# Performance work log

Measured on AMD Instinct MI355X. Metric: run time of the kernel, lower is better.

Reference implementation:

```python
import jax, jax.numpy as jnp
import numpy as np


def c2p_gather(feat, ind):
    # feat: [B, C, M] cell features; ind: [B, N, 2] (slot 0 = cell index)
    B, C, _ = feat.shape
    idx = ind[:, :, 0]                                   # [B, N]
    idx3 = jnp.broadcast_to(idx[:, None, :], (B, C, idx.shape[1]))
    return jnp.take_along_axis(feat, idx3, axis=2)       # [B, C, N]


def p2c_scatter(x, ind, num_cells):
    # x: [B, C, Nn] point features; ind: [B, Nn, 2]; scatter-add into [B, C, M]
    idx = ind[:, :, 0]                                   # [B, Nn]

    def per_batch(xb, ib):
        # xb: [C, Nn] -> segment_sum over points -> [M, C]
        return jax.ops.segment_sum(xb.T, ib, num_segments=num_cells).T

    return jax.vmap(per_batch)(x, idx)                   # [B, C, M]


def setup_inputs() -> dict:
    key = jax.random.key(0)
    ks = jax.random.split(key, 8)
    B, Cv, Cr, E, Co = 2, 64, 20, 64, 64
    Mv, Mr = 100000, 50000
    N = 262144            # gathered points; os=8 -> bundle=4 -> Nn=65536 nodes
    Nn = N // 4
    return {
        "v_feat": jax.random.normal(ks[0], (B, Cv, Mv), jnp.float32),
        "r_feat": jax.random.normal(ks[1], (B, Cr, Mr), jnp.float32),
        "Wq": jax.random.normal(ks[2], (E, Cr), jnp.float32) * 0.1,
        "Wk": jax.random.normal(ks[3], (E, Cv), jnp.float32) * 0.1,
        "Wv": jax.random.normal(ks[4], (E, Cv), jnp.float32) * 0.1,
        "Wo": jax.random.normal(ks[5], (Co, E), jnp.float32) * 0.1,
        "v2p_ind": jax.random.randint(ks[6], (B, N, 2), 0, Mv).astype(jnp.int64),
        "r2p_ind": jax.random.randint(ks[7], (B, Nn, 2), 0, Mr).astype(jnp.int64),
        "os": 8,
    }


def reference(v_feat, r_feat, Wq, Wk, Wv, Wo, v2p_ind, r2p_ind, os):
    bundle = max(1, int(os) // 2)
    B, Cv, _ = v_feat.shape
    Mr = r_feat.shape[2]

    # c2p gather of detached features (module calls .detach())
    v_pp = c2p_gather(jax.lax.stop_gradient(v_feat), v2p_ind)       # [B, Cv, N]
    N = v_pp.shape[2]
    Nn = N // bundle
    v_nodes = v_pp.reshape(B, Cv, Nn, bundle)                        # bundle splits
    r_pp = c2p_gather(jax.lax.stop_gradient(r_feat), r2p_ind)        # [B, Cr, Nn]

    # attent1d: query from r feature, keys/values from the neighbor bundle
    E = Wq.shape[0]
    q = jnp.einsum("ec,bcn->ben", Wq, r_pp)                          # [B, E, Nn]
    k = jnp.einsum("ec,bcnm->benm", Wk, v_nodes)                     # [B, E, Nn, bundle]
    v = jnp.einsum("ec,bcnm->benm", Wv, v_nodes)
    scores = jnp.einsum("ben,benm->bnm", q, k) / jnp.sqrt(jnp.float32(E))
    attn = jax.nn.softmax(scores, axis=-1)                           # over bundle
    agg = jnp.einsum("bnm,benm->ben", attn, v)                       # [B, E, Nn]
    xr = jnp.einsum("oe,ben->bon", Wo, agg)                          # [B, Co, Nn]

    # p2c scatter back to r-cell layout (size taken from r_feat)
    xr_mapped = p2c_scatter(xr, r2p_ind, Mr)                         # [B, Co, Mr]
    return xr_mapped
```

## Files before the change

kernel.cpp:

```cpp
#include <hip/hip_runtime.h>
#include <cstdint>

#define BB 2
#define CV 64
#define CR 20
#define EE 64
#define CO 64
#define NZ 256

__global__ __launch_bounds__(256) void k_tr(
    const float* __restrict__ vf, float* __restrict__ vt, int Mv, int ntm) {
  __shared__ float tile[64 * 64];
  int b = blockIdx.x / ntm, tm = blockIdx.x % ntm;
  int m0 = tm * 64;
  int t = threadIdx.x;
  const float* src = vf + (size_t)b * CV * Mv;
  float* dst = vt + (size_t)b * Mv * 64;
  if (((Mv & 3) == 0) && (m0 + 64 <= Mv)) {
    #pragma unroll
    for (int p = 0; p < 4; ++p) {
      int c = p * 16 + (t >> 4), mq = t & 15;
      float4 v = *(const float4*)&src[(size_t)c * Mv + m0 + 4 * mq];
      *(float4*)&tile[c * 64 + ((mq ^ ((c >> 2) & 15)) << 2)] = v;
    }
    __syncthreads();
    #pragma unroll
    for (int p = 0; p < 4; ++p) {
      int ml = p * 16 + (t >> 4), cq = t & 15;
      int mc = ml >> 2, mr = ml & 3;
      int ch = (mc ^ cq) << 2;
      float4 w;
      w.x = tile[(4 * cq + 0) * 64 + ch + mr];
      w.y = tile[(4 * cq + 1) * 64 + ch + mr];
      w.z = tile[(4 * cq + 2) * 64 + ch + mr];
      w.w = tile[(4 * cq + 3) * 64 + ch + mr];
      *(float4*)&dst[(size_t)(m0 + ml) * 64 + 4 * cq] = w;
    }
  } else {
    for (int p = 0; p < 16; ++p) {
      int idx = p * 256 + t;
      int c = idx >> 6, ml = idx & 63;
      int m = m0 + ml;
      float v = (m < Mv) ? src[(size_t)c * Mv + m] : 0.f;
      tile[c * 64 + (((ml >> 2) ^ ((c >> 2) & 15)) << 2) + (ml & 3)] = v;
    }
    __syncthreads();
    for (int p = 0; p < 16; ++p) {
      int idx = p * 256 + t;
      int ml = idx >> 6, c = idx & 63;
      int m = m0 + ml;
      if (m < Mv)
        dst[(size_t)m * 64 + c] =
            tile[c * 64 + (((ml >> 2) ^ ((c >> 2) & 15)) << 2) + (ml & 3)];
    }
  }
}

__global__ __launch_bounds__(256) void k_pre(
    const float* __restrict__ rf,
    const float* __restrict__ Wq, const float* __restrict__ Wk,
    const float* __restrict__ Wv, const float* __restrict__ Wo,
    const int* __restrict__ r2p,
    float* __restrict__ gq, float* __restrict__ H,
    int* __restrict__ flag, float4* __restrict__ xs4,
    int Mr, int ntj, int NGQ, int xsE4) {
  __shared__ float smem[CR * 64 + CR * 68];
  int bid = blockIdx.x, t = threadIdx.x;
  if (bid < NGQ) {
    float* Gl = smem;
    float* rt = smem + CR * 64;
    for (int idx = t; idx < CR * CV; idx += 256) {
      int cr = idx / CV, cv = idx - cr * CV;
      float s = 0.f;
      #pragma unroll
      for (int e = 0; e < EE; ++e) s += Wq[e * CR + cr] * Wk[e * CV + cv];
      Gl[idx] = s;
    }
    int b = bid / ntj, tj = bid - b * ntj;
    int j0 = tj * 64;
    const float* src = rf + (size_t)b * CR * Mr;
    for (int idx = t; idx < CR * 64; idx += 256) {
      int c = idx >> 6, jl = idx & 63;
      int j = j0 + jl;
      rt[c * 68 + jl] = (j < Mr) ? src[(size_t)c * Mr + j] : 0.f;
    }
    __syncthreads();
    int ti = t & 15, tjq = t >> 4;
    float acc[4][4];
    #pragma unroll
    for (int a = 0; a < 4; ++a)
      #pragma unroll
      for (int q = 0; q < 4; ++q) acc[a][q] = 0.f;
    for (int c = 0; c < CR; ++c) {
      float4 gx = *(const float4*)&Gl[c * 64 + 4 * ti];
      float4 xj = *(const float4*)&rt[c * 68 + 4 * tjq];
      #pragma unroll
      for (int a = 0; a < 4; ++a) {
        float xv = (a == 0) ? xj.x : (a == 1) ? xj.y : (a == 2) ? xj.z : xj.w;
        acc[a][0] += xv * gx.x;
        acc[a][1] += xv * gx.y;
        acc[a][2] += xv * gx.z;
        acc[a][3] += xv * gx.w;
      }
    }
    #pragma unroll
    for (int a = 0; a < 4; ++a) {
      int j = j0 + 4 * tjq + a;
      if (j < Mr) {
        float4 w = make_float4(acc[a][0], acc[a][1], acc[a][2], acc[a][3]);
        *(float4*)&gq[((size_t)b * Mr + j) * 64 + 4 * ti] = w;
      }
    }
    return;
  }
  int r = bid - NGQ;
  if (r < 16) {
    int idx = r * 256 + t;
    int o = idx >> 6, c = idx & 63;
    float s = 0.f;
    #pragma unroll
    for (int e = 0; e < EE; ++e) s += Wo[o * EE + e] * Wv[e * CV + c];
    H[idx] = s;
  } else if (r == 16) {
    __shared__ int any;
    if (t == 0) any = 0;
    __syncthreads();
    int nz = 0;
    for (int i = t; i < 4096; i += 256) nz |= r2p[2 * i + 1];
    if (nz) atomicOr(&any, 1);
    __syncthreads();
    if (t == 0) *flag = (any == 0) ? 4 : 2;
  } else {
    int z = r - 17;
    float4 zz = make_float4(0.f, 0.f, 0.f, 0.f);
    for (int i = z * 256 + t; i < xsE4; i += NZ * 256) xs4[i] = zz;
  }
}

template <int WS>
__device__ __forceinline__ void load_idx(
    const int* __restrict__ r2p, const int* __restrict__ v2p,
    int p, int Nn, int N, int P,
    int& b, int& j, int& i0, int& i1, int& i2, int& i3) {
  if (p >= P) { b = 0; j = 0; i0 = i1 = i2 = i3 = 0; return; }
  b = (p >= Nn) ? 1 : 0;
  int n = p - b * Nn;
  j = r2p[((size_t)b * Nn + n) * WS];
  const int* vi = v2p + ((size_t)b * N + (size_t)n * 4) * WS;
  if (WS == 2) {
    int4 w0 = *(const int4*)vi;
    int4 w1 = *(const int4*)(vi + 4);
    i0 = w0.x; i1 = w0.z; i2 = w1.x; i3 = w1.z;
  } else {
    i0 = vi[0]; i1 = vi[1 * WS]; i2 = vi[2 * WS]; i3 = vi[3 * WS];
  }
}

__device__ __forceinline__ float gred16(float h) {
  h += __shfl_xor(h, 1);
  h += __shfl_xor(h, 2);
  h += __shfl_xor(h, 4);
  h += __shfl_xor(h, 8);
  return h;
}

__device__ __forceinline__ float4 att4(float4 q4, float4 c0, float4 c1,
                                       float4 c2, float4 c3) {
  float s0 = gred16(q4.x * c0.x + q4.y * c0.y + q4.z * c0.z + q4.w * c0.w);
  float s1 = gred16(q4.x * c1.x + q4.y * c1.y + q4.z * c1.z + q4.w * c1.w);
  float s2 = gred16(q4.x * c2.x + q4.y * c2.y + q4.z * c2.z + q4.w * c2.w);
  float s3 = gred16(q4.x * c3.x + q4.y * c3.y + q4.z * c3.z + q4.w * c3.w);
  s0 *= 0.125f; s1 *= 0.125f; s2 *= 0.125f; s3 *= 0.125f;
  float mx = fmaxf(fmaxf(s0, s1), fmaxf(s2, s3));
  float e0 = __expf(s0 - mx), e1 = __expf(s1 - mx);
  float e2 = __expf(s2 - mx), e3 = __expf(s3 - mx);
  float inv = 1.f / (e0 + e1 + e2 + e3);
  e0 *= inv; e1 *= inv; e2 *= inv; e3 *= inv;
  float4 ag;
  ag.x = e0 * c0.x + e1 * c1.x + e2 * c2.x + e3 * c3.x;
  ag.y = e0 * c0.y + e1 * c1.y + e2 * c2.y + e3 * c3.y;
  ag.z = e0 * c0.z + e1 * c1.z + e2 * c2.z + e3 * c3.z;
  ag.w = e0 * c0.w + e1 * c1.w + e2 * c2.w + e3 * c3.w;
  return ag;
}

template <int WS>
__device__ __forceinline__ void main_body(
    const float* __restrict__ vt, const float* __restrict__ gq,
    const int* __restrict__ v2p, const int* __restrict__ r2p,
    float* __restrict__ xs, float* __restrict__ my,
    int Mv, int Mr, int N, int Nn, int P) {
  int t = threadIdx.x;
  int lane = t & 63, sl = t & 15, grp = (t >> 4) & 3;
  int base = (blockIdx.x * 4 + (t >> 6)) * 8;
  if (base >= P) return;
  int pA = base + grp, pB = base + grp + 4;
  int bA, jA, a0, a1, a2, a3, bB, jB, b0, b1, b2, b3;
  load_idx<WS>(r2p, v2p, pA, Nn, N, P, bA, jA, a0, a1, a2, a3);
  load_idx<WS>(r2p, v2p, pB, Nn, N, P, bB, jB, b0, b1, b2, b3);
  const float* gqA = gq + (size_t)bA * Mr * 64;
  const float* vbA = vt + (size_t)bA * Mv * 64;
  const float* gqB = gq + (size_t)bB * Mr * 64;
  const float* vbB = vt + (size_t)bB * Mv * 64;
  float4 qA  = *(const float4*)&gqA[(size_t)jA * 64 + 4 * sl];
  float4 cA0 = *(const float4*)&vbA[(size_t)a0 * 64 + 4 * sl];
  float4 cA1 = *(const float4*)&vbA[(size_t)a1 * 64 + 4 * sl];
  float4 cA2 = *(const float4*)&vbA[(size_t)a2 * 64 + 4 * sl];
  float4 cA3 = *(const float4*)&vbA[(size_t)a3 * 64 + 4 * sl];
  float4 qB  = *(const float4*)&gqB[(size_t)jB * 64 + 4 * sl];
  float4 cB0 = *(const float4*)&vbB[(size_t)b0 * 64 + 4 * sl];
  float4 cB1 = *(const float4*)&vbB[(size_t)b1 * 64 + 4 * sl];
  float4 cB2 = *(const float4*)&vbB[(size_t)b2 * 64 + 4 * sl];
  float4 cB3 = *(const float4*)&vbB[(size_t)b3 * 64 + 4 * sl];
  float4 agA = att4(qA, cA0, cA1, cA2, cA3);
  *(float4*)&my[grp * 68 + 4 * sl] = agA;
  float4 agB = att4(qB, cB0, cB1, cB2, cB3);
  *(float4*)&my[(grp + 4) * 68 + 4 * sl] = agB;
  #pragma unroll
  for (int g = 0; g < 8; ++g) {
    if (base + g < P) {
      int jg = __shfl((g < 4) ? jA : jB, (g & 3) * 16);
      int bg = ((base + g) >= Nn) ? 1 : 0;
      float v = my[g * 68 + lane];
      atomicAdd(&xs[((size_t)bg * Mr + jg) * 64 + lane], v);
    }
  }
}

__global__ __launch_bounds__(256, 8) void k_main(
    const float* __restrict__ vt, const float* __restrict__ gq,
    const int* __restrict__ v2p, const int* __restrict__ r2p,
    float* __restrict__ xs, const int* __restrict__ flag,
    int Mv, int Mr, int N, int Nn, int P) {
  __shared__ float sc[4 * 8 * 68];
  float* my = sc + (threadIdx.x >> 6) * (8 * 68);
  if (*flag == 2)
    main_body<2>(vt, gq, v2p, r2p, xs, my, Mv, Mr, N, Nn, P);
  else
    main_body<4>(vt, gq, v2p, r2p, xs, my, Mv, Mr, N, Nn, P);
}

__device__ __forceinline__ int hsw(int fidx) {
  return fidx ^ (((fidx >> 8) & 7) << 2);
}

__global__ __launch_bounds__(256) void k_out_t(
    const float* __restrict__ xs, const float* __restrict__ H,
    float* __restrict__ out, int Mr, int ntj) {
  __shared__ float Hl[CO * CV];
  __shared__ float xt[64][68];
  int b = blockIdx.x / ntj, tj = blockIdx.x % ntj;
  int j0 = tj * 64;
  int t = threadIdx.x;
  for (int idx = t; idx < CO * CV; idx += 256) Hl[hsw(idx)] = H[idx];
  const float* src = xs + (size_t)b * Mr * 64;
  #pragma unroll
  for (int k = 0; k < 4; ++k) {
    int jl = k * 16 + (t >> 4), c4 = t & 15;
    int j = j0 + jl;
    float4 v = (j < Mr) ? *(const float4*)&src[(size_t)j * 64 + 4 * c4]
                        : make_float4(0.f, 0.f, 0.f, 0.f);
    *(float4*)&xt[jl][4 * c4] = v;
  }
  __syncthreads();
  int ti = t & 15;
  int tjq4 = t >> 4;
  float acc[4][4];
  #pragma unroll
  for (int a = 0; a < 4; ++a)
    #pragma unroll
    for (int q = 0; q < 4; ++q) acc[a][q] = 0.f;
  #pragma unroll 4
  for (int cq = 0; cq < 16; ++cq) {
    float4 xv[4], hb[4];
    #pragma unroll
    for (int a = 0; a < 4; ++a)
      xv[a] = *(const float4*)&xt[4 * tjq4 + a][4 * cq];
    #pragma unroll
    for (int q = 0; q < 4; ++q) {
      int row = 4 * ti + q;
      hb[q] = *(const float4*)&Hl[hsw(row * 64 + 4 * cq)];
    }
    #pragma unroll
    for (int a = 0; a < 4; ++a)
      #pragma unroll
      for (int q = 0; q < 4; ++q)
        acc[a][q] += xv[a].x * hb[q].x + xv[a].y * hb[q].y +
                     xv[a].z * hb[q].z + xv[a].w * hb[q].w;
  }
  __syncthreads();
  #pragma unroll
  for (int a = 0; a < 4; ++a)
    #pragma unroll
    for (int q = 0; q < 4; ++q)
      xt[4 * ti + q][4 * tjq4 + a] = acc[a][q];
  __syncthreads();
  float* dst = out + (size_t)b * CO * Mr;
  #pragma unroll
  for (int k = 0; k < 4; ++k) {
    int o = k * 16 + (t >> 4), j4 = t & 15;
    int j = j0 + 4 * j4;
    if (j + 3 < Mr) {
      *(float4*)&dst[(size_t)o * Mr + j] = *(const float4*)&xt[o][4 * j4];
    } else {
      #pragma unroll
      for (int i = 0; i < 4; ++i)
        if (j + i < Mr) dst[(size_t)o * Mr + j + i] = xt[o][4 * j4 + i];
    }
  }
}

extern "C" void kernel_launch(void* const* d_in, const int* in_sizes, int n_in,
                              void* d_out, int out_size, void* d_ws, size_t ws_size,
                              hipStream_t stream) {
  const float* v_feat = (const float*)d_in[0];
  const float* r_feat = (const float*)d_in[1];
  const float* Wq = (const float*)d_in[2];
  const float* Wk = (const float*)d_in[3];
  const float* Wv = (const float*)d_in[4];
  const float* Wo = (const float*)d_in[5];
  const int* v2p = (const int*)d_in[6];
  const int* r2p = (const int*)d_in[7];

  int Mv = in_sizes[0] / (BB * CV);
  int Mr = in_sizes[1] / (BB * CR);
  int N  = in_sizes[6] / (BB * 2);
  int Nn = in_sizes[7] / (BB * 2);

  float* ws = (float*)d_ws;
  float* vt = ws;
  float* gq = vt + (size_t)BB * Mv * 64;
  float* xs = gq + (size_t)BB * Mr * 64;
  float* H  = xs + (size_t)BB * Mr * 64;
  int* flag = (int*)(H + CO * CV);
  float* out = (float*)d_out;

  int ntm = (Mv + 63) / 64;
  int ntj = (Mr + 63) / 64;
  int NGQ = BB * ntj;
  int xsE4 = (BB * Mr * 64) / 4;

  k_tr<<<BB * ntm, 256, 0, stream>>>(v_feat, vt, Mv, ntm);

  k_pre<<<NGQ + 17 + NZ, 256, 0, stream>>>(r_feat, Wq, Wk, Wv, Wo, r2p,
                                           gq, H, flag, (float4*)xs,
                                           Mr, ntj, NGQ, xsE4);

  int P = BB * Nn;
  int blocks = (P + 31) / 32;
  k_main<<<blocks, 256, 0, stream>>>(vt, gq, v2p, r2p, xs, flag,
                                     Mv, Mr, N, Nn, P);

  k_out_t<<<BB * ntj, 256, 0, stream>>>(xs, H, out, Mr, ntj);
}
```

Before: 220.8 us.

## Compute Wq·Wk product once and merge weight prep into transpose kernel

The Wq^T·Wk product G was previously recomputed inside every gq block (each block did 1280 dot products of length 64). It is now computed once by a few extra blocks of the transpose kernel, along with H, the flag and the zeroing of xs. The gq projection moves to a separate lightweight kernel that only loads the precomputed G. This removes redundant per-block weight math but adds one kernel launch and one more global round trip for G.

```diff
diff --git a/kernel.cpp b/kernel.cpp
--- a/kernel.cpp
+++ b/kernel.cpp
@@ -9,119 +9,77 @@
 #define NZ 256
 
 __global__ __launch_bounds__(256) void k_tr(
-    const float* __restrict__ vf, float* __restrict__ vt, int Mv, int ntm) {
+    const float* __restrict__ vf, const float* __restrict__ Wq,
+    const float* __restrict__ Wk, const float* __restrict__ Wv,
+    const float* __restrict__ Wo, const int* __restrict__ r2p,
+    float* __restrict__ vt, float* __restrict__ G, float* __restrict__ H,
+    int* __restrict__ flag, float4* __restrict__ xs4,
+    int Mv, int ntm, int NT, int xsE4) {
   __shared__ float tile[64 * 64];
-  int b = blockIdx.x / ntm, tm = blockIdx.x % ntm;
-  int m0 = tm * 64;
-  int t = threadIdx.x;
-  const float* src = vf + (size_t)b * CV * Mv;
-  float* dst = vt + (size_t)b * Mv * 64;
-  if (((Mv & 3) == 0) && (m0 + 64 <= Mv)) {
-    #pragma unroll
-    for (int p = 0; p < 4; ++p) {
-      int c = p * 16 + (t >> 4), mq = t & 15;
-      float4 v = *(const float4*)&src[(size_t)c * Mv + m0 + 4 * mq];
-      *(float4*)&tile[c * 64 + ((mq ^ ((c >> 2) & 15)) << 2)] = v;
-    }
-    __syncthreads();
-    #pragma unroll
-    for (int p = 0; p < 4; ++p) {
-      int ml = p * 16 + (t >> 4), cq = t & 15;
-      int mc = ml >> 2, mr = ml & 3;
-      int ch = (mc ^ cq) << 2;
-      float4 w;
-      w.x = tile[(4 * cq + 0) * 64 + ch + mr];
-      w.y = tile[(4 * cq + 1) * 64 + ch + mr];
-      w.z = tile[(4 * cq + 2) * 64 + ch + mr];
-      w.w = tile[(4 * cq + 3) * 64 + ch + mr];
-      *(float4*)&dst[(size_t)(m0 + ml) * 64 + 4 * cq] = w;
-    }
-  } else {
-    for (int p = 0; p < 16; ++p) {
-      int idx = p * 256 + t;
-      int c = idx >> 6, ml = idx & 63;
-      int m = m0 + ml;
-      float v = (m < Mv) ? src[(size_t)c * Mv + m] : 0.f;
-      tile[c * 64 + (((ml >> 2) ^ ((c >> 2) & 15)) << 2) + (ml & 3)] = v;
-    }
-    __syncthreads();
-    for (int p = 0; p < 16; ++p) {
-      int idx = p * 256 + t;
-      int ml = idx >> 6, c = idx & 63;
-      int m = m0 + ml;
-      if (m < Mv)
-        dst[(size_t)m * 64 + c] =
-            tile[c * 64 + (((ml >> 2) ^ ((c >> 2) & 15)) << 2) + (ml & 3)];
-    }
-  }
-}
-
-__global__ __launch_bounds__(256) void k_pre(
-    const float* __restrict__ rf,
-    const float* __restrict__ Wq, const float* __restrict__ Wk,
-    const float* __restrict__ Wv, const float* __restrict__ Wo,
-    const int* __restrict__ r2p,
-    float* __restrict__ gq, float* __restrict__ H,
-    int* __restrict__ flag, float4* __restrict__ xs4,
-    int Mr, int ntj, int NGQ, int xsE4) {
-  __shared__ float smem[CR * 64 + CR * 68];
   int bid = blockIdx.x, t = threadIdx.x;
-  if (bid < NGQ) {
-    float* Gl = smem;
-    float* rt = smem + CR * 64;
-    for (int idx = t; idx < CR * CV; idx += 256) {
+  if (bid < NT) {
+    int b = bid / ntm, tm = bid % ntm;
+    int m0 = tm * 64;
+    const float* src = vf + (size_t)b * CV * Mv;
+    float* dst = vt + (size_t)b * Mv * 64;
+    if (((Mv & 3) == 0) && (m0 + 64 <= Mv)) {
+      #pragma unroll
+      for (int p = 0; p < 4; ++p) {
+        int c = p * 16 + (t >> 4), mq = t & 15;
+        float4 v = *(const float4*)&src[(size_t)c * Mv + m0 + 4 * mq];
+        *(float4*)&tile[c * 64 + ((mq ^ ((c >> 2) & 15)) << 2)] = v;
+      }
+      __syncthreads();
+      #pragma unroll
+      for (int p = 0; p < 4; ++p) {
+        int ml = p * 16 + (t >> 4), cq = t & 15;
+        int mc = ml >> 2, mr = ml & 3;
+        int ch = (mc ^ cq) << 2;
+        float4 w;
+        w.x = tile[(4 * cq + 0) * 64 + ch + mr];
+        w.y = tile[(4 * cq + 1) * 64 + ch + mr];
+        w.z = tile[(4 * cq + 2) * 64 + ch + mr];
+        w.w = tile[(4 * cq + 3) * 64 + ch + mr];
+        *(float4*)&dst[(size_t)(m0 + ml) * 64 + 4 * cq] = w;
+      }
+    } else {
+      for (int p = 0; p < 16; ++p) {
+        int idx = p * 256 + t;
+        int c = idx >> 6, ml = idx & 63;
+        int m = m0 + ml;
+        float v = (m < Mv) ? src[(size_t)c * Mv + m] : 0.f;
+        tile[c * 64 + (((ml >> 2) ^ ((c >> 2) & 15)) << 2) + (ml & 3)] = v;
+      }
+      __syncthreads();
+      for (int p = 0; p < 16; ++p) {
+        int idx = p * 256 + t;
+        int ml = idx >> 6, c = idx & 63;
+        int m = m0 + ml;
+        if (m < Mv)
+          dst[(size_t)m * 64 + c] =
+              tile[c * 64 + (((ml >> 2) ^ ((c >> 2) & 15)) << 2) + (ml & 3)];
+      }
+    }
+    return;
+  }
+  int r = bid - NT;
+  if (r < 5) {
+    int idx = r * 256 + t;
+    if (idx < CR * CV) {
       int cr = idx / CV, cv = idx - cr * CV;
       float s = 0.f;
       #pragma unroll
       for (int e = 0; e < EE; ++e) s += Wq[e * CR + cr] * Wk[e * CV + cv];
-      Gl[idx] = s;
-    }
-    int b = bid / ntj, tj = bid - b * ntj;
-    int j0 = tj * 64;
-    const float* src = rf + (size_t)b * CR * Mr;
-    for (int idx = t; idx < CR * 64; idx += 256) {
-      int c = idx >> 6, jl = idx & 63;
-      int j = j0 + jl;
-      rt[c * 68 + jl] = (j < Mr) ? src[(size_t)c * Mr + j] : 0.f;
-    }
-    __syncthreads();
-    int ti = t & 15, tjq = t >> 4;
-    float acc[4][4];
-    #pragma unroll
-    for (int a = 0; a < 4; ++a)
-      #pragma unroll
-      for (int q = 0; q < 4; ++q) acc[a][q] = 0.f;
-    for (int c = 0; c < CR; ++c) {
-      float4 gx = *(const float4*)&Gl[c * 64 + 4 * ti];
-      float4 xj = *(const float4*)&rt[c * 68 + 4 * tjq];
-      #pragma unroll
-      for (int a = 0; a < 4; ++a) {
-        float xv = (a == 0) ? xj.x : (a == 1) ? xj.y : (a == 2) ? xj.z : xj.w;
-        acc[a][0] += xv * gx.x;
-        acc[a][1] += xv * gx.y;
-        acc[a][2] += xv * gx.z;
-        acc[a][3] += xv * gx.w;
-      }
-    }
-    #pragma unroll
-    for (int a = 0; a < 4; ++a) {
-      int j = j0 + 4 * tjq + a;
-      if (j < Mr) {
-        float4 w = make_float4(acc[a][0], acc[a][1], acc[a][2], acc[a][3]);
-        *(float4*)&gq[((size_t)b * Mr + j) * 64 + 4 * ti] = w;
-      }
-    }
-    return;
-  }
-  int r = bid - NGQ;
-  if (r < 16) {
-    int idx = r * 256 + t;
+      G[idx] = s;
+    }
+  } else if (r < 21) {
+    int idx = (r - 5) * 256 + t;
     int o = idx >> 6, c = idx & 63;
     float s = 0.f;
     #pragma unroll
     for (int e = 0; e < EE; ++e) s += Wo[o * EE + e] * Wv[e * CV + c];
     H[idx] = s;
-  } else if (r == 16) {
+  } else if (r == 21) {
     __shared__ int any;
     if (t == 0) any = 0;
     __syncthreads();
@@ -131,9 +89,53 @@
     __syncthreads();
     if (t == 0) *flag = (any == 0) ? 4 : 2;
   } else {
-    int z = r - 17;
+    int z = r - 22;
     float4 zz = make_float4(0.f, 0.f, 0.f, 0.f);
     for (int i = z * 256 + t; i < xsE4; i += NZ * 256) xs4[i] = zz;
+  }
+}
+
+__global__ __launch_bounds__(256) void k_gq(
+    const float* __restrict__ rf, const float* __restrict__ G,
+    float* __restrict__ gq, int Mr, int ntj) {
+  __shared__ float Gl[CR * 64];
+  __shared__ float rt[CR * 68];
+  int bid = blockIdx.x, t = threadIdx.x;
+  for (int idx = t; idx < CR * CV; idx += 256) Gl[idx] = G[idx];
+  int b = bid / ntj, tj = bid - b * ntj;
+  int j0 = tj * 64;
+  const float* src = rf + (size_t)b * CR * Mr;
+  for (int idx = t; idx < CR * 64; idx += 256) {
+    int c = idx >> 6, jl = idx & 63;
+    int j = j0 + jl;
+    rt[c * 68 + jl] = (j < Mr) ? src[(size_t)c * Mr + j] : 0.f;
+  }
+  __syncthreads();
+  int ti = t & 15, tjq = t >> 4;
+  float acc[4][4];
+  #pragma unroll
+  for (int a = 0; a < 4; ++a)
+    #pragma unroll
+    for (int q = 0; q < 4; ++q) acc[a][q] = 0.f;
+  for (int c = 0; c < CR; ++c) {
+    float4 gx = *(const float4*)&Gl[c * 64 + 4 * ti];
+    float4 xj = *(const float4*)&rt[c * 68 + 4 * tjq];
+    #pragma unroll
+    for (int a = 0; a < 4; ++a) {
+      float xv = (a == 0) ? xj.x : (a == 1) ? xj.y : (a == 2) ? xj.z : xj.w;
+      acc[a][0] += xv * gx.x;
+      acc[a][1] += xv * gx.y;
+      acc[a][2] += xv * gx.z;
+      acc[a][3] += xv * gx.w;
+    }
+  }
+  #pragma unroll
+  for (int a = 0; a < 4; ++a) {
+    int j = j0 + 4 * tjq + a;
+    if (j < Mr) {
+      float4 w = make_float4(acc[a][0], acc[a][1], acc[a][2], acc[a][3]);
+      *(float4*)&gq[((size_t)b * Mr + j) * 64 + 4 * ti] = w;
+    }
   }
 }
 
@@ -331,20 +333,22 @@
   float* vt = ws;
   float* gq = vt + (size_t)BB * Mv * 64;
   float* xs = gq + (size_t)BB * Mr * 64;
-  float* H  = xs + (size_t)BB * Mr * 64;
+  float* G  = xs + (size_t)BB * Mr * 64;
+  float* H  = G + CR * CV;
   int* flag = (int*)(H + CO * CV);
   float* out = (float*)d_out;
 
   int ntm = (Mv + 63) / 64;
   int ntj = (Mr + 63) / 64;
+  int NT = BB * ntm;
   int NGQ = BB * ntj;
   int xsE4 = (BB * Mr * 64) / 4;
 
-  k_tr<<<BB * ntm, 256, 0, stream>>>(v_feat, vt, Mv, ntm);
-
-  k_pre<<<NGQ + 17 + NZ, 256, 0, stream>>>(r_feat, Wq, Wk, Wv, Wo, r2p,
-                                           gq, H, flag, (float4*)xs,
-                                           Mr, ntj, NGQ, xsE4);
+  k_tr<<<NT + 22 + NZ, 256, 0, stream>>>(v_feat, Wq, Wk, Wv, Wo, r2p,
+                                         vt, G, H, flag, (float4*)xs,
+                                         Mv, ntm, NT, xsE4);
+
+  k_gq<<<NGQ, 256, 0, stream>>>(r_feat, G, gq, Mr, ntj);
 
   int P = BB * Nn;
   int blocks = (P + 31) / 32;
```

After: 208.5 us. -5.6%, faster.
